# Performance work log

Measured on AMD Instinct MI355X. Metric: run time of the kernel, lower is better.

The kernel has to match this reference:

```python
import jax, jax.numpy as jnp
import numpy as np

B, S, V = 64, 2048, 256

def setup_inputs() -> dict:
    key = jax.random.key(0)
    k1, k2 = jax.random.split(key)
    logits = jax.random.normal(k1, (B, S, V), dtype=jnp.float32)
    prior_knowledge_matrix = jax.random.normal(k2, (V, V), dtype=jnp.float32)
    return {"logits": logits, "prior_knowledge_matrix": prior_knowledge_matrix}

def reference(logits, prior_knowledge_matrix):
    # log-softmax over tag dim
    d = jax.nn.log_softmax(logits, axis=-1)  # [B, S, V]
    # out[b, i] = d[b, i, :] @ M @ d[b, i+1, :]  for i in [0, S-2]
    # fused diagonal-only bilinear form over adjacent positions
    left = jnp.einsum('bsv,vw->bsw', d[:, :-1, :], prior_knowledge_matrix)  # [B, S-1, V]
    out = jnp.einsum('bsw,bsw->bs', left, d[:, 1:, :])  # [B, S-1]
    return out
```

## Files before the change

### kernel.cpp

```cpp
#include <hip/hip_runtime.h>
#include <hip/hip_bf16.h>


#define BQ   64
#define ROWS (BQ + 1)
#define LDA  264
#define PF   6

typedef __attribute__((ext_vector_type(8))) short short8;
typedef __attribute__((ext_vector_type(4))) float f32x4;

__device__ __forceinline__ unsigned short f2bf(float f) {
    unsigned int u = __float_as_uint(f);
    unsigned int r = (u + 0x7fffu + ((u >> 16) & 1u)) >> 16;
    return (unsigned short)r;
}
__device__ __forceinline__ float bf2f(unsigned short u) {
    return __uint_as_float(((unsigned int)u) << 16);
}

__global__ void pk_prep(const float* __restrict__ M, unsigned short* __restrict__ mt) {
    int idx = blockIdx.x * 256 + threadIdx.x;
    int n = idx >> 8, k = idx & 255;
    mt[idx] = f2bf(M[k * 256 + n]);
}

__global__ __launch_bounds__(256, 4) void pk_main(const float* __restrict__ logits,
                                                  const unsigned short* __restrict__ mt,
                                                  float* __restrict__ out) {
    __shared__ unsigned short dA[ROWS * LDA];
    __shared__ float partial[BQ][4];

    const int tid  = threadIdx.x;
    const int lane = tid & 63;
    const int wid  = tid >> 6;
    const int b     = blockIdx.x >> 5;
    const int chunk = blockIdx.x & 31;
    const int i0    = chunk * BQ;
    const int nrows = min(ROWS, 2048 - i0);

    const int l15 = lane & 15;
    const int kg  = (lane >> 4) * 8;
    const unsigned short* mw = mt + ((size_t)(wid * 64 + l15)) * 256 + kg;

    {
        const float* base = logits + ((size_t)(b * 2048 + i0)) * 256 + lane * 4;
        float4 buf[PF];
        #pragma unroll
        for (int p = 0; p < PF; ++p) {
            int row = wid + 4 * p;
            if (row < nrows) buf[p] = *reinterpret_cast<const float4*>(base + (size_t)row * 256);
        }
        #pragma unroll
        for (int j = 0; j < 17; ++j) {
            int row = wid + 4 * j;
            if (row < nrows) {
                float4 x = buf[j % PF];
                int prow = wid + 4 * (j + PF);
                if (prow < nrows)
                    buf[j % PF] = *reinterpret_cast<const float4*>(base + (size_t)prow * 256);
                float s = __expf(x.x) + __expf(x.y) + __expf(x.z) + __expf(x.w);
                #pragma unroll
                for (int off = 32; off; off >>= 1) s += __shfl_xor(s, off);
                float lse = __logf(s);
                ushort4 pk;
                pk.x = f2bf(x.x - lse); pk.y = f2bf(x.y - lse);
                pk.z = f2bf(x.z - lse); pk.w = f2bf(x.w - lse);
                *reinterpret_cast<ushort4*>(&dA[row * LDA + lane * 4]) = pk;
            }
        }
    }

    f32x4 acc[4][4];
    #pragma unroll
    for (int a = 0; a < 4; ++a)
        #pragma unroll
        for (int n = 0; n < 4; ++n) acc[a][n] = (f32x4){0.f, 0.f, 0.f, 0.f};

    short8 bA[4], bB[4];
    #pragma unroll
    for (int n = 0; n < 4; ++n)
        bA[n] = *reinterpret_cast<const short8*>(mw + n * 16 * 256);

    __syncthreads();

    #pragma unroll
    for (int kt = 0; kt < 8; ++kt) {
        short8* cur = (kt & 1) ? bB : bA;
        short8* nxt = (kt & 1) ? bA : bB;
        if (kt < 7) {
            #pragma unroll
            for (int n = 0; n < 4; ++n)
                nxt[n] = *reinterpret_cast<const short8*>(mw + n * 16 * 256 + (kt + 1) * 32);
        }
        short8 aF[4];
        #pragma unroll
        for (int a = 0; a < 4; ++a)
            aF[a] = *reinterpret_cast<const short8*>(&dA[(a * 16 + l15) * LDA + kt * 32 + kg]);
        #pragma unroll
        for (int a = 0; a < 4; ++a)
            #pragma unroll
            for (int n = 0; n < 4; ++n)
                acc[a][n] = __builtin_amdgcn_mfma_f32_16x16x32_bf16(aF[a], cur[n], acc[a][n], 0, 0, 0);
    }

    const int rg = lane >> 4;
    #pragma unroll
    for (int a = 0; a < 4; ++a) {
        #pragma unroll
        for (int r2 = 0; r2 < 4; ++r2) {
            int row = a * 16 + rg * 4 + r2;
            float p = 0.f;
            #pragma unroll
            for (int n = 0; n < 4; ++n) {
                int col = wid * 64 + n * 16 + l15;
                p += acc[a][n][r2] * bf2f(dA[(row + 1) * LDA + col]);
            }
            #pragma unroll
            for (int off = 8; off; off >>= 1) p += __shfl_xor(p, off);
            if (l15 == 0) partial[row][wid] = p;
        }
    }
    __syncthreads();

    if (tid < BQ) {
        float4 pv = *reinterpret_cast<const float4*>(partial[tid]);
        int i = i0 + tid;
        if (i < 2047) out[(size_t)b * 2047 + i] = pv.x + pv.y + pv.z + pv.w;
    }
}

extern "C" void kernel_launch(void* const* d_in, const int* in_sizes, int n_in,
                              void* d_out, int out_size, void* d_ws, size_t ws_size,
                              hipStream_t stream) {
    const float* logits = (const float*)d_in[0];
    const float* M      = (const float*)d_in[1];
    float* out          = (float*)d_out;
    unsigned short* mt  = (unsigned short*)d_ws;

    pk_prep<<<256, 256, 0, stream>>>(M, mt);
    pk_main<<<64 * 32, 256, 0, stream>>>(logits, mt, out);
}
```

Measured before the change: 220.0 us.

## Halve rows per block and issue all logit loads upfront with 16-lane rows

The per-block row tile drops from 64 to 32, so the grid doubles and the launch bounds target 6 blocks per CU, using the smaller shared-memory footprint for higher occupancy. The log-softmax prologue is restructured: each row is now handled by 16 lanes, so a wave covers four rows at once with a 4-step shuffle reduction. All of a thread's logit loads are issued before any compute, replacing the rolling prefetch buffer. In exchange, every block still reads all of the bf16 matrix for half as many rows, which doubles matrix-fragment traffic from L2. The extra overlap row is also re-read more often.

```diff
diff --git a/kernel.cpp b/kernel.cpp
--- a/kernel.cpp
+++ b/kernel.cpp
@@ -2,10 +2,9 @@
 #include <hip/hip_bf16.h>
 
 
-#define BQ   64
+#define BQ   32
 #define ROWS (BQ + 1)
 #define LDA  264
-#define PF   6
 
 typedef __attribute__((ext_vector_type(8))) short short8;
 typedef __attribute__((ext_vector_type(4))) float f32x4;
@@ -25,7 +24,7 @@
     mt[idx] = f2bf(M[k * 256 + n]);
 }
 
-__global__ __launch_bounds__(256, 4) void pk_main(const float* __restrict__ logits,
+__global__ __launch_bounds__(256, 6) void pk_main(const float* __restrict__ logits,
                                                   const unsigned short* __restrict__ mt,
                                                   float* __restrict__ out) {
     __shared__ unsigned short dA[ROWS * LDA];
@@ -34,8 +33,8 @@
     const int tid  = threadIdx.x;
     const int lane = tid & 63;
     const int wid  = tid >> 6;
-    const int b     = blockIdx.x >> 5;
-    const int chunk = blockIdx.x & 31;
+    const int b     = blockIdx.x >> 6;
+    const int chunk = blockIdx.x & 63;
     const int i0    = chunk * BQ;
     const int nrows = min(ROWS, 2048 - i0);
 
@@ -44,36 +43,79 @@
     const unsigned short* mw = mt + ((size_t)(wid * 64 + l15)) * 256 + kg;
 
     {
-        const float* base = logits + ((size_t)(b * 2048 + i0)) * 256 + lane * 4;
-        float4 buf[PF];
+        const int sub = lane >> 4;
+        const float* rowbase = logits + ((size_t)(b * 2048 + i0)) * 256 + l15 * 4;
+        const int r0 = wid * 4 + sub;
+        const int r1 = 16 + wid * 4 + sub;
+        const int r2b = 32 + wid * 4 + sub;
+        const bool has2 = (r2b < nrows);
+
+        float4 x0[4], x1[4], x2[4];
         #pragma unroll
-        for (int p = 0; p < PF; ++p) {
-            int row = wid + 4 * p;
-            if (row < nrows) buf[p] = *reinterpret_cast<const float4*>(base + (size_t)row * 256);
+        for (int p = 0; p < 4; ++p)
+            x0[p] = *reinterpret_cast<const float4*>(rowbase + (size_t)r0 * 256 + p * 64);
+        #pragma unroll
+        for (int p = 0; p < 4; ++p)
+            x1[p] = *reinterpret_cast<const float4*>(rowbase + (size_t)r1 * 256 + p * 64);
+        if (has2) {
+            #pragma unroll
+            for (int p = 0; p < 4; ++p)
+                x2[p] = *reinterpret_cast<const float4*>(rowbase + (size_t)r2b * 256 + p * 64);
         }
-        #pragma unroll
-        for (int j = 0; j < 17; ++j) {
-            int row = wid + 4 * j;
-            if (row < nrows) {
-                float4 x = buf[j % PF];
-                int prow = wid + 4 * (j + PF);
-                if (prow < nrows)
-                    buf[j % PF] = *reinterpret_cast<const float4*>(base + (size_t)prow * 256);
-                float s = __expf(x.x) + __expf(x.y) + __expf(x.z) + __expf(x.w);
-                #pragma unroll
-                for (int off = 32; off; off >>= 1) s += __shfl_xor(s, off);
-                float lse = __logf(s);
+
+        {
+            float s = 0.f;
+            #pragma unroll
+            for (int p = 0; p < 4; ++p)
+                s += __expf(x0[p].x) + __expf(x0[p].y) + __expf(x0[p].z) + __expf(x0[p].w);
+            #pragma unroll
+            for (int off = 8; off; off >>= 1) s += __shfl_xor(s, off);
+            float lse = __logf(s);
+            #pragma unroll
+            for (int p = 0; p < 4; ++p) {
                 ushort4 pk;
-                pk.x = f2bf(x.x - lse); pk.y = f2bf(x.y - lse);
-                pk.z = f2bf(x.z - lse); pk.w = f2bf(x.w - lse);
-                *reinterpret_cast<ushort4*>(&dA[row * LDA + lane * 4]) = pk;
+                pk.x = f2bf(x0[p].x - lse); pk.y = f2bf(x0[p].y - lse);
+                pk.z = f2bf(x0[p].z - lse); pk.w = f2bf(x0[p].w - lse);
+                *reinterpret_cast<ushort4*>(&dA[r0 * LDA + l15 * 4 + p * 64]) = pk;
+            }
+        }
+        {
+            float s = 0.f;
+            #pragma unroll
+            for (int p = 0; p < 4; ++p)
+                s += __expf(x1[p].x) + __expf(x1[p].y) + __expf(x1[p].z) + __expf(x1[p].w);
+            #pragma unroll
+            for (int off = 8; off; off >>= 1) s += __shfl_xor(s, off);
+            float lse = __logf(s);
+            #pragma unroll
+            for (int p = 0; p < 4; ++p) {
+                ushort4 pk;
+                pk.x = f2bf(x1[p].x - lse); pk.y = f2bf(x1[p].y - lse);
+                pk.z = f2bf(x1[p].z - lse); pk.w = f2bf(x1[p].w - lse);
+                *reinterpret_cast<ushort4*>(&dA[r1 * LDA + l15 * 4 + p * 64]) = pk;
+            }
+        }
+        if (has2) {
+            float s = 0.f;
+            #pragma unroll
+            for (int p = 0; p < 4; ++p)
+                s += __expf(x2[p].x) + __expf(x2[p].y) + __expf(x2[p].z) + __expf(x2[p].w);
+            #pragma unroll
+            for (int off = 8; off; off >>= 1) s += __shfl_xor(s, off);
+            float lse = __logf(s);
+            #pragma unroll
+            for (int p = 0; p < 4; ++p) {
+                ushort4 pk;
+                pk.x = f2bf(x2[p].x - lse); pk.y = f2bf(x2[p].y - lse);
+                pk.z = f2bf(x2[p].z - lse); pk.w = f2bf(x2[p].w - lse);
+                *reinterpret_cast<ushort4*>(&dA[r2b * LDA + l15 * 4 + p * 64]) = pk;
             }
         }
     }
 
-    f32x4 acc[4][4];
+    f32x4 acc[2][4];
     #pragma unroll
-    for (int a = 0; a < 4; ++a)
+    for (int a = 0; a < 2; ++a)
         #pragma unroll
         for (int n = 0; n < 4; ++n) acc[a][n] = (f32x4){0.f, 0.f, 0.f, 0.f};
 
@@ -93,12 +135,12 @@
             for (int n = 0; n < 4; ++n)
                 nxt[n] = *reinterpret_cast<const short8*>(mw + n * 16 * 256 + (kt + 1) * 32);
         }
-        short8 aF[4];
+        short8 aF[2];
         #pragma unroll
-        for (int a = 0; a < 4; ++a)
+        for (int a = 0; a < 2; ++a)
             aF[a] = *reinterpret_cast<const short8*>(&dA[(a * 16 + l15) * LDA + kt * 32 + kg]);
         #pragma unroll
-        for (int a = 0; a < 4; ++a)
+        for (int a = 0; a < 2; ++a)
             #pragma unroll
             for (int n = 0; n < 4; ++n)
                 acc[a][n] = __builtin_amdgcn_mfma_f32_16x16x32_bf16(aF[a], cur[n], acc[a][n], 0, 0, 0);
@@ -106,7 +148,7 @@
 
     const int rg = lane >> 4;
     #pragma unroll
-    for (int a = 0; a < 4; ++a) {
+    for (int a = 0; a < 2; ++a) {
         #pragma unroll
         for (int r2 = 0; r2 < 4; ++r2) {
             int row = a * 16 + rg * 4 + r2;
@@ -139,5 +181,5 @@
     unsigned short* mt  = (unsigned short*)d_ws;
 
     pk_prep<<<256, 256, 0, stream>>>(M, mt);
-    pk_main<<<64 * 32, 256, 0, stream>>>(logits, mt, out);
+    pk_main<<<64 * 64, 256, 0, stream>>>(logits, mt, out);
 }
```

After: 233.0 us. 5.9% more time.
